# Kernel optimization log

Measured on AMD Instinct MI355X. Metric: run time of the kernel, lower is better.

Reference implementation:

```python
import jax, jax.numpy as jnp
import numpy as np

B, N, D = 8, 8192, 64          # batch, input points, point feature dim
NPOINT, NSAMPLE = 1024, 16     # FPS samples S, KNN neighbors K
WN, OUT = 16, 128              # weightnet out channels, output channels
CIN = 3 + D                    # concat(xyz_norm, point feats) = linear in_channel
NEG_SLOPE = 0.1


def setup_inputs() -> dict:
    key = jax.random.key(0)
    ks = jax.random.split(key, 8)
    rn = lambda k, shp, s: jax.random.normal(k, shp, jnp.float32) * s
    return {
        "xyz": rn(ks[0], (B, 3, N), 1.0),
        "points": rn(ks[1], (B, D, N), 1.0),
        "w1": rn(ks[2], (3, 8), 0.5), "b1": jnp.zeros((8,), jnp.float32),
        "w2": rn(ks[3], (8, 8), 0.35), "b2": jnp.zeros((8,), jnp.float32),
        "w3": rn(ks[4], (8, WN), 0.35), "b3": jnp.zeros((WN,), jnp.float32),
        "lin_w": rn(ks[5], (WN * CIN, OUT), 0.03),
        "lin_b": jnp.zeros((OUT,), jnp.float32),
    }


def _fps(xyz):
    """Furthest point sampling. xyz: [B,N,3] -> idx [B,NPOINT] int32."""
    def step(carry, _):
        dist, farthest = carry  # [B,N], [B]
        centroid = jnp.take_along_axis(xyz, farthest[:, None, None], axis=1)  # [B,1,3]
        d = jnp.sum((xyz - centroid) ** 2, axis=-1)  # [B,N]
        dist = jnp.minimum(dist, d)
        return (dist, jnp.argmax(dist, axis=-1).astype(jnp.int32)), farthest
    init = (jnp.full((xyz.shape[0], xyz.shape[1]), 1e10, xyz.dtype),
            jnp.zeros((xyz.shape[0],), jnp.int32))
    _, idxs = jax.lax.scan(step, init, None, length=NPOINT)
    return idxs.T  # [B, NPOINT]


def reference(xyz, points, w1, b1, w2, b2, w3, b3, lin_w, lin_b):
    xyz_t = xyz.transpose(0, 2, 1)       # [B,N,3]
    pts_t = points.transpose(0, 2, 1)    # [B,N,D]

    fps_idx = _fps(xyz_t)                                   # [B,S]
    bidx = jnp.arange(B)[:, None]
    new_xyz = xyz_t[bidx, fps_idx]                          # [B,S,3]

    # KNN: squared distances (same ordering as euclidean cdist)
    sqr = jnp.sum((new_xyz[:, :, None, :] - xyz_t[:, None, :, :]) ** 2, axis=-1)  # [B,S,N]
    _, knn = jax.lax.top_k(-sqr, NSAMPLE)                   # [B,S,K]

    b3i = jnp.arange(B)[:, None, None]
    g_xyz = xyz_t[b3i, knn]                                 # [B,S,K,3]
    g_xyz_norm = g_xyz - new_xyz[:, :, None, :]             # [B,S,K,3]
    g_pts = pts_t[b3i, knn]                                 # [B,S,K,D]
    feat = jnp.concatenate([g_xyz_norm, g_pts], axis=-1)    # [B,S,K,3+D]

    # WeightNet: 1x1 convs == per-neighbor MLP on xyz offsets
    h = jax.nn.relu(g_xyz_norm @ w1 + b1)
    h = jax.nn.relu(h @ w2 + b2)
    wts = jax.nn.relu(h @ w3 + b3)                          # [B,S,K,WN]

    # weighted aggregation over K, then flatten [C, WN]
    agg = jnp.einsum('bskc,bskw->bscw', feat, wts).reshape(B, NPOINT, CIN * WN)
    out = agg @ lin_w + lin_b                               # [B,S,OUT]
    out = jnp.where(out > 0, out, NEG_SLOPE * out)          # LeakyReLU(0.1)

    return new_xyz.transpose(0, 2, 1), out.transpose(0, 2, 1), fps_idx
```

## Files before the change

### kernel.cpp

```cpp
#include <hip/hip_runtime.h>
#include <hip/hip_bf16.h>

#define NPTS   8192
#define NBATCH 8
#define S      1024
#define K      16
#define D      64
#define CIN    67
#define WN     16
#define OUTC   128

#define OUT_MAIN 24576
#define OUT_FPS  1073152

#define T_FPS   0
#define T_TP    8
#define T_KNN   1032
#define T_FEAT  1544
#define T_GEMM  2568
#define NBLK    2824

typedef float v2f __attribute__((ext_vector_type(2)));

struct Ctrl {
  int ticket;
  int pad0[15];
  int progress[8];
  int knn_prefix[8];
  int tp_done[8];
  int pad1[8];
  int tile_done[128];
};

__device__ __forceinline__ void wait_ge(int* p, int need) {
  if (threadIdx.x == 0)
    while (__hip_atomic_load(p, __ATOMIC_ACQUIRE, __HIP_MEMORY_SCOPE_AGENT) < need)
      __builtin_amdgcn_s_sleep(2);
  __syncthreads();
}

template <int CTRL, int RM>
__device__ __forceinline__ unsigned long long dpp_max_step(unsigned long long key) {
  int lo = __builtin_amdgcn_update_dpp(0, (int)(unsigned)(key & 0xFFFFFFFFull), CTRL, RM, 0xF, true);
  int hi = __builtin_amdgcn_update_dpp(0, (int)(unsigned)(key >> 32),           CTRL, RM, 0xF, true);
  unsigned long long o = ((unsigned long long)(unsigned)hi << 32) | (unsigned)lo;
  return o > key ? o : key;
}

__device__ void fps_role(int b, const float* __restrict__ xyz, float4* __restrict__ nx4,
                         float* __restrict__ out, Ctrl* ctrl, void* smem)
{
#pragma clang fp contract(off)
  float* s_x = (float*)smem;
  float* s_y = s_x + NPTS;
  float* s_z = s_y + NPTS;
  float4* hist = (float4*)((char*)smem + 98304);
  unsigned long long* slots = (unsigned long long*)((char*)smem + 114688);

  const int tid  = threadIdx.x;
  const int wave = tid >> 6;
  const int lane = tid & 63;
  const float* xb = xyz + (size_t)b * 3 * NPTS;

  v2f px[8], py[8], pz[8], dist[8];
#pragma unroll
  for (int p = 0; p < 8; p++) {
    int ne = (2 * p) * 512 + tid;
    int no = ne + 512;
    px[p] = (v2f){xb[ne], xb[no]};
    py[p] = (v2f){xb[NPTS + ne], xb[NPTS + no]};
    pz[p] = (v2f){xb[2 * NPTS + ne], xb[2 * NPTS + no]};
    dist[p] = (v2f){1e10f, 1e10f};
    s_x[ne] = px[p].x; s_x[no] = px[p].y;
    s_y[ne] = py[p].x; s_y[no] = py[p].y;
    s_z[ne] = pz[p].x; s_z[no] = pz[p].y;
  }

  int far = 0;
  float cx = xb[0], cy = xb[NPTS], cz = xb[2 * NPTS];

  for (int t = 0; t < 1024; t++) {
    if (tid == (t & 511))
      hist[t] = make_float4(cx, cy, cz, (float)far);

    if ((t & 31) == 0 && t > 0 && wave == 0 && lane < 32) {
      int tt = t - 32 + lane;
      float4 h = hist[tt];
      nx4[(b << 10) + tt] = h;
      __threadfence();
      if (lane == 0)
        __hip_atomic_store(&ctrl->progress[b], t, __ATOMIC_RELEASE, __HIP_MEMORY_SCOPE_AGENT);
    }

    const v2f c2x = (v2f){cx, cx}, c2y = (v2f){cy, cy}, c2z = (v2f){cz, cz};

    float bd_e = -1.0f, bd_o = -1.0f;
    int   ce   = 0,     co   = 0;
#pragma unroll
    for (int p = 0; p < 8; p++) {
      v2f dx = px[p] - c2x, dy = py[p] - c2y, dz = pz[p] - c2z;
      v2f d  = (dx * dx + dy * dy) + dz * dz;
      float nde = fminf(dist[p].x, d.x);
      float ndo = fminf(dist[p].y, d.y);
      dist[p].x = nde;
      dist[p].y = ndo;
      if (nde > bd_e) { bd_e = nde; ce = 2 * p; }
      if (ndo > bd_o) { bd_o = ndo; co = 2 * p + 1; }
    }

    unsigned long long ke =
        ((unsigned long long)__float_as_uint(bd_e) << 32) | (unsigned)(~(unsigned)(ce * 512 + tid));
    unsigned long long ko =
        ((unsigned long long)__float_as_uint(bd_o) << 32) | (unsigned)(~(unsigned)(co * 512 + tid));
    unsigned long long key = ko > ke ? ko : ke;

    key = dpp_max_step<0x111, 0xF>(key);
    key = dpp_max_step<0x112, 0xF>(key);
    key = dpp_max_step<0x114, 0xF>(key);
    key = dpp_max_step<0x118, 0xF>(key);
    key = dpp_max_step<0x142, 0xA>(key);
    key = dpp_max_step<0x143, 0xC>(key);
    if (lane == 63) slots[(t & 1) * 8 + wave] = key;
    __syncthreads();

    const unsigned long long* sl = slots + (t & 1) * 8;
    unsigned long long k0 = sl[0], k1 = sl[1], k2 = sl[2], k3 = sl[3];
    unsigned long long k4 = sl[4], k5 = sl[5], k6 = sl[6], k7 = sl[7];
    k0 = k1 > k0 ? k1 : k0;
    k2 = k3 > k2 ? k3 : k2;
    k4 = k5 > k4 ? k5 : k4;
    k6 = k7 > k6 ? k7 : k6;
    k0 = k2 > k0 ? k2 : k0;
    k4 = k6 > k4 ? k6 : k4;
    k0 = k4 > k0 ? k4 : k0;
    int gi = (int)(~(unsigned)(k0 & 0xFFFFFFFFull));
    far = gi;
    cx = s_x[gi]; cy = s_y[gi]; cz = s_z[gi];
  }
  __syncthreads();

  if (wave == 0 && lane < 32) {
    int tt = 992 + lane;
    float4 h = hist[tt];
    nx4[(b << 10) + tt] = h;
    __threadfence();
    if (lane == 0)
      __hip_atomic_store(&ctrl->progress[b], 1024, __ATOMIC_RELEASE, __HIP_MEMORY_SCOPE_AGENT);
  }

#pragma unroll
  for (int j = 0; j < 2; j++) {
    int t = j * 512 + tid;
    float4 h = hist[t];
    out[OUT_FPS + b * 1024 + t] = h.w;
    out[b * 3072 + t]           = h.x;
    out[b * 3072 + 1024 + t]    = h.y;
    out[b * 3072 + 2048 + t]    = h.z;
  }
}

__device__ void tp_role(int bid, const float* __restrict__ pts, float* __restrict__ ptt,
                        Ctrl* ctrl, void* smem)
{
  float* tile = (float*)smem;
  const int b  = bid >> 7;
  const int n0 = (bid & 127) * 64;
  const float* pb = pts + (size_t)b * D * NPTS;
#pragma unroll
  for (int i = 0; i < 8; i++) {
    int s = threadIdx.x + i * 512;
    int nl = s & 63, d = s >> 6;
    tile[d * 65 + nl] = pb[(size_t)d * NPTS + n0 + nl];
  }
  __syncthreads();
  float* ob = ptt + ((size_t)b * NPTS + n0) * D;
#pragma unroll
  for (int i = 0; i < 8; i++) {
    int s = threadIdx.x + i * 512;
    int dl = s & 63, nl = s >> 6;
    ob[(size_t)nl * D + dl] = tile[dl * 65 + nl];
  }
  __syncthreads();
  if (threadIdx.x == 0) {
    __threadfence();
    __hip_atomic_fetch_add(&ctrl->tp_done[b], 1, __ATOMIC_RELEASE, __HIP_MEMORY_SCOPE_AGENT);
  }
}

__device__ void knn_role(int kidx, const float* __restrict__ xyz, const float4* __restrict__ nx4,
                         int* __restrict__ knn, Ctrl* ctrl, void* smem)
{
#pragma clang fp contract(off)
  unsigned long long (*s_k)[544] = (unsigned long long (*)[544])smem;
  const int tid   = threadIdx.x;
  const int cl    = tid >> 5;
  const int chunk = tid & 31;
  const int b     = kidx >> 6;
  const int c0    = (kidx & 63) * 16;
  const int csel  = (b << 10) + c0 + cl;

  wait_ge(&ctrl->progress[b], c0 + 16);

  const float* xb = xyz + (size_t)b * 3 * NPTS;
  const float4 c4 = nx4[csel];
  const float cx = c4.x, cy = c4.y, cz = c4.z;

  float nd[16]; int ni[16];
#pragma unroll
  for (int k = 0; k < 16; k++) { nd[k] = 3.4e38f; ni[k] = 0x7FFFFFFF; }

  for (int jj = 0; jj < 256; jj++) {
    int j = jj * 32 + chunk;
    float dx = xb[j] - cx, dy = xb[NPTS + j] - cy, dz = xb[2 * NPTS + j] - cz;
    float d  = (dx * dx + dy * dy) + dz * dz;
    float cv = d; int iv = j;
#pragma unroll
    for (int k = 0; k < 16; k++) {
      bool sw = cv < nd[k];
      float tv = nd[k]; int ti = ni[k];
      nd[k] = sw ? cv : tv;  ni[k] = sw ? iv : ti;
      cv    = sw ? tv : cv;  iv    = sw ? ti : iv;
    }
  }
#pragma unroll
  for (int k = 0; k < 16; k++)
    s_k[cl][chunk * 17 + k] =
        ((unsigned long long)__float_as_uint(nd[k]) << 32) | (unsigned)ni[k];
  s_k[cl][chunk * 17 + 16] = ~0ull;
  __syncthreads();

  if (tid < 16) {
    int pos[32];
#pragma unroll
    for (int c = 0; c < 32; c++) pos[c] = 0;
    for (int r = 0; r < 16; r++) {
      unsigned long long bk = ~0ull; int bc = 0;
#pragma unroll
      for (int c = 0; c < 32; c++) {
        unsigned long long kv = s_k[tid][c * 17 + pos[c]];
        if (kv < bk) { bk = kv; bc = c; }
      }
#pragma unroll
      for (int c = 0; c < 32; c++) pos[c] += (c == bc);
      knn[(size_t)((b << 10) + c0 + tid) * 16 + r] = (int)(bk & 0xFFFFFFFFull);
    }
  }
  __syncthreads();
  if (tid == 0) {
    __threadfence();
    while (__hip_atomic_load(&ctrl->knn_prefix[b], __ATOMIC_ACQUIRE, __HIP_MEMORY_SCOPE_AGENT) < c0)
      __builtin_amdgcn_s_sleep(2);
    __hip_atomic_store(&ctrl->knn_prefix[b], c0 + 16, __ATOMIC_RELEASE, __HIP_MEMORY_SCOPE_AGENT);
  }
}

__device__ void feat_role(int fidx, const float* __restrict__ xyz, const float4* __restrict__ nx4,
                          const float* __restrict__ ptt, const int* __restrict__ knn,
                          const float* __restrict__ w1, const float* __restrict__ b1,
                          const float* __restrict__ w2, const float* __restrict__ b2,
                          const float* __restrict__ w3, const float* __restrict__ b3,
                          float* __restrict__ agg, Ctrl* ctrl, void* smem)
{
  float* s_wts = (float*)smem;
  float* s_off = s_wts + 8 * 272;
  int*   s_nk  = (int*)(s_off + 8 * 48);

  const int C0 = fidx * 8;
  const int b  = C0 >> 10;
  const int c0l = C0 & 1023;

  wait_ge(&ctrl->knn_prefix[b], c0l + 8);
  wait_ge(&ctrl->tp_done[b], 128);

  const int wv   = threadIdx.x >> 6;
  const int lane = threadIdx.x & 63;
  const int csel = C0 + wv;

  if (lane < 16) {
    int nk = knn[(size_t)csel * 16 + lane];
    s_nk[wv * 16 + lane] = nk;
    const float* xb = xyz + (size_t)b * 3 * NPTS;
    const float4 c4 = nx4[csel];
    float ox = xb[nk]            - c4.x;
    float oy = xb[NPTS + nk]     - c4.y;
    float oz = xb[2 * NPTS + nk] - c4.z;
    s_off[wv * 48 + lane * 3 + 0] = ox;
    s_off[wv * 48 + lane * 3 + 1] = oy;
    s_off[wv * 48 + lane * 3 + 2] = oz;
    float h1[8], h2[8];
#pragma unroll
    for (int j = 0; j < 8; j++)
      h1[j] = fmaxf(0.f, ox * w1[j] + oy * w1[8 + j] + oz * w1[16 + j] + b1[j]);
#pragma unroll
    for (int j = 0; j < 8; j++) {
      float a = b2[j];
#pragma unroll
      for (int i = 0; i < 8; i++) a = fmaf(h1[i], w2[i * 8 + j], a);
      h2[j] = fmaxf(0.f, a);
    }
#pragma unroll
    for (int w = 0; w < 16; w++) {
      float a = b3[w];
#pragma unroll
      for (int i = 0; i < 8; i++) a = fmaf(h2[i], w3[i * 16 + w], a);
      s_wts[wv * 272 + lane * 17 + w] = fmaxf(0.f, a);
    }
  }
  __syncthreads();

  float f[16];
#pragma unroll
  for (int k = 0; k < 16; k++) {
    int nk = s_nk[wv * 16 + k];
    f[k] = ptt[((size_t)b * NPTS + nk) * D + lane];
  }

  float acc[16];
#pragma unroll
  for (int w = 0; w < 16; w++) acc[w] = 0.f;
#pragma unroll
  for (int k = 0; k < 16; k++) {
#pragma unroll
    for (int w = 0; w < 16; w++)
      acc[w] = fmaf(f[k], s_wts[wv * 272 + k * 17 + w], acc[w]);
  }
  float* arow = agg + (size_t)csel * (CIN * WN) + (3 + lane) * 16;
#pragma unroll
  for (int q = 0; q < 4; q++) {
    float4 v = make_float4(acc[4 * q], acc[4 * q + 1], acc[4 * q + 2], acc[4 * q + 3]);
    *(float4*)(arow + 4 * q) = v;
  }

  if (lane < 48) {
    int c = lane >> 4, w = lane & 15;
    float a = 0.f;
#pragma unroll
    for (int k = 0; k < 16; k++)
      a = fmaf(s_off[wv * 48 + k * 3 + c], s_wts[wv * 272 + k * 17 + w], a);
    agg[(size_t)csel * (CIN * WN) + c * 16 + w] = a;
  }
  __syncthreads();
  if (threadIdx.x == 0) {
    __threadfence();
    __hip_atomic_fetch_add(&ctrl->tile_done[C0 >> 6], 1, __ATOMIC_RELEASE, __HIP_MEMORY_SCOPE_AGENT);
  }
}

__device__ void gemm_role(int gidx, const float* __restrict__ agg, const float* __restrict__ lin_w,
                          const float* __restrict__ lin_b, float* __restrict__ out,
                          Ctrl* ctrl, void* smem)
{
  float* a_t = (float*)smem;
  float* b_t = a_t + 16 * 68;
  const int rt   = gidx >> 1;
  const int ct   = gidx & 1;
  const int row0 = rt * 64;
  const int c0   = ct * 64;

  wait_ge(&ctrl->tile_done[rt], 8);

  const int tid = threadIdx.x;
  const int cg  = tid & 31;
  const int rg  = tid >> 5;

  float acc[4][2] = {};
  for (int kt = 0; kt < 67; kt++) {
    const int k0 = kt * 16;
#pragma unroll
    for (int i = 0; i < 2; i++) {
      int s = tid + i * 512;
      int kk = s & 15, r = s >> 4;
      a_t[kk * 68 + r] = agg[(size_t)(row0 + r) * (CIN * WN) + k0 + kk];
    }
#pragma unroll
    for (int i = 0; i < 2; i++) {
      int s = tid + i * 512;
      int c = s & 63, kk = s >> 6;
      b_t[kk * 64 + c] = lin_w[(size_t)(k0 + kk) * OUTC + c0 + c];
    }
    __syncthreads();
#pragma unroll
    for (int kk = 0; kk < 16; kk++) {
      const float4 a0 = *(const float4*)&a_t[kk * 68 + rg * 4];
      float bv0 = b_t[kk * 64 + cg * 2];
      float bv1 = b_t[kk * 64 + cg * 2 + 1];
      float av[4] = {a0.x, a0.y, a0.z, a0.w};
#pragma unroll
      for (int rr = 0; rr < 4; rr++) {
        acc[rr][0] = fmaf(av[rr], bv0, acc[rr][0]);
        acc[rr][1] = fmaf(av[rr], bv1, acc[rr][1]);
      }
    }
    __syncthreads();
  }
#pragma unroll
  for (int rr = 0; rr < 4; rr++) {
#pragma unroll
    for (int cc = 0; cc < 2; cc++) {
      int R = row0 + rg * 4 + rr;
      int C = c0 + cg * 2 + cc;
      float v = acc[rr][cc] + lin_b[C];
      v = v > 0.f ? v : 0.1f * v;
      int bb = R >> 10, ss = R & 1023;
      out[OUT_MAIN + ((size_t)(bb * OUTC + C)) * 1024 + ss] = v;
    }
  }
}

__global__ __launch_bounds__(512)
void mega_kernel(const float* __restrict__ xyz, const float* __restrict__ pts,
                 const float* __restrict__ w1, const float* __restrict__ b1,
                 const float* __restrict__ w2, const float* __restrict__ b2,
                 const float* __restrict__ w3, const float* __restrict__ b3,
                 const float* __restrict__ lin_w, const float* __restrict__ lin_b,
                 float* __restrict__ out, float4* __restrict__ nx4,
                 int* __restrict__ knn, float* __restrict__ ptt,
                 float* __restrict__ agg, Ctrl* ctrl)
{
  __shared__ __align__(16) unsigned long long smem[14400];
  __shared__ int s_ticket;
  if (threadIdx.x == 0)
    s_ticket = __hip_atomic_fetch_add(&ctrl->ticket, 1, __ATOMIC_RELAXED, __HIP_MEMORY_SCOPE_AGENT);
  __syncthreads();
  const int tk = s_ticket;

  if (tk < T_TP)
    fps_role(tk, xyz, nx4, out, ctrl, smem);
  else if (tk < T_KNN)
    tp_role(tk - T_TP, pts, ptt, ctrl, smem);
  else if (tk < T_FEAT)
    knn_role(tk - T_KNN, xyz, nx4, knn, ctrl, smem);
  else if (tk < T_GEMM)
    feat_role(tk - T_FEAT, xyz, nx4, ptt, knn, w1, b1, w2, b2, w3, b3, agg, ctrl, smem);
  else
    gemm_role(tk - T_GEMM, agg, lin_w, lin_b, out, ctrl, smem);
}

extern "C" void kernel_launch(void* const* d_in, const int* in_sizes, int n_in,
                              void* d_out, int out_size, void* d_ws, size_t ws_size,
                              hipStream_t stream) {
  const float* xyz    = (const float*)d_in[0];
  const float* points = (const float*)d_in[1];
  const float* w1     = (const float*)d_in[2];
  const float* b1     = (const float*)d_in[3];
  const float* w2     = (const float*)d_in[4];
  const float* b2     = (const float*)d_in[5];
  const float* w3     = (const float*)d_in[6];
  const float* b3     = (const float*)d_in[7];
  const float* lin_w  = (const float*)d_in[8];
  const float* lin_b  = (const float*)d_in[9];
  float* out = (float*)d_out;
  char*  ws  = (char*)d_ws;

  float4* nx4  = (float4*)(ws);
  int*    knn  = (int*)   (ws + 131072);
  Ctrl*   ctrl = (Ctrl*)  (ws + 655360);
  float*  ptt  = (float*) (ws + 1048576);
  float*  agg  = (float*) (ws + 17825792);

  hipMemsetAsync(ctrl, 0, 4096, stream);
  mega_kernel<<<NBLK, 512, 0, stream>>>(xyz, points, w1, b1, w2, b2, w3, b3,
                                        lin_w, lin_b, out, nx4, knn, ptt, agg, ctrl);
}
```

Baseline: 1.543 ms.

## Replace progress counters with self-validating 64-bit data flags for FPS/KNN handoff

FPS results and KNN indices are now published as packed 64-bit relaxed atomic words with a nonzero sentinel (index+1), so consumers poll the data directly instead of waiting on progress counters and the serialized knn_prefix chain. This removes the thread fences and the in-order KNN prefix publication, letting feature blocks start as soon as their own neighbors are ready. The cost is a larger memset of the workspace, per-lane spinning on data, and reliance on relaxed atomics for ordering. Ordering on the nxA word relies on the x/y floats not both being zero, which is a subtle correctness risk.

```diff
diff --git a/kernel.cpp b/kernel.cpp
--- a/kernel.cpp
+++ b/kernel.cpp
@@ -20,22 +20,28 @@
 #define T_GEMM  2568
 #define NBLK    2824
 
+#define SCOPE __HIP_MEMORY_SCOPE_AGENT
+
 typedef float v2f __attribute__((ext_vector_type(2)));
 
 struct Ctrl {
   int ticket;
-  int pad0[15];
-  int progress[8];
-  int knn_prefix[8];
+  int pad0[31];
   int tp_done[8];
-  int pad1[8];
+  int pad1[24];
   int tile_done[128];
 };
 
-__device__ __forceinline__ void wait_ge(int* p, int need) {
+__device__ __forceinline__ unsigned long long aload64(const unsigned long long* p) {
+  return __hip_atomic_load(p, __ATOMIC_RELAXED, SCOPE);
+}
+__device__ __forceinline__ void astore64(unsigned long long* p, unsigned long long v) {
+  __hip_atomic_store(p, v, __ATOMIC_RELAXED, SCOPE);
+}
+__device__ __forceinline__ void wait_cnt(int* p, int need) {
   if (threadIdx.x == 0)
-    while (__hip_atomic_load(p, __ATOMIC_ACQUIRE, __HIP_MEMORY_SCOPE_AGENT) < need)
-      __builtin_amdgcn_s_sleep(2);
+    while (__hip_atomic_load(p, __ATOMIC_RELAXED, SCOPE) < need)
+      __builtin_amdgcn_s_sleep(4);
   __syncthreads();
 }
 
@@ -47,8 +53,10 @@
   return o > key ? o : key;
 }
 
-__device__ void fps_role(int b, const float* __restrict__ xyz, float4* __restrict__ nx4,
-                         float* __restrict__ out, Ctrl* ctrl, void* smem)
+__device__ void fps_role(int b, const float* __restrict__ xyz,
+                         unsigned long long* __restrict__ nxA,
+                         unsigned long long* __restrict__ nxB,
+                         float* __restrict__ out, void* smem)
 {
 #pragma clang fp contract(off)
   float* s_x = (float*)smem;
@@ -86,10 +94,11 @@
     if ((t & 31) == 0 && t > 0 && wave == 0 && lane < 32) {
       int tt = t - 32 + lane;
       float4 h = hist[tt];
-      nx4[(b << 10) + tt] = h;
-      __threadfence();
-      if (lane == 0)
-        __hip_atomic_store(&ctrl->progress[b], t, __ATOMIC_RELEASE, __HIP_MEMORY_SCOPE_AGENT);
+      int gidx = (b << 10) + tt;
+      astore64(&nxA[gidx],
+               ((unsigned long long)__float_as_uint(h.x) << 32) | __float_as_uint(h.y));
+      astore64(&nxB[gidx],
+               ((unsigned long long)__float_as_uint(h.z) << 32) | (unsigned)((int)h.w + 1));
     }
 
     const v2f c2x = (v2f){cx, cx}, c2y = (v2f){cy, cy}, c2z = (v2f){cz, cz};
@@ -142,10 +151,11 @@
   if (wave == 0 && lane < 32) {
     int tt = 992 + lane;
     float4 h = hist[tt];
-    nx4[(b << 10) + tt] = h;
-    __threadfence();
-    if (lane == 0)
-      __hip_atomic_store(&ctrl->progress[b], 1024, __ATOMIC_RELEASE, __HIP_MEMORY_SCOPE_AGENT);
+    int gidx = (b << 10) + tt;
+    astore64(&nxA[gidx],
+             ((unsigned long long)__float_as_uint(h.x) << 32) | __float_as_uint(h.y));
+    astore64(&nxB[gidx],
+             ((unsigned long long)__float_as_uint(h.z) << 32) | (unsigned)((int)h.w + 1));
   }
 
 #pragma unroll
@@ -181,29 +191,37 @@
     ob[(size_t)nl * D + dl] = tile[dl * 65 + nl];
   }
   __syncthreads();
-  if (threadIdx.x == 0) {
-    __threadfence();
-    __hip_atomic_fetch_add(&ctrl->tp_done[b], 1, __ATOMIC_RELEASE, __HIP_MEMORY_SCOPE_AGENT);
-  }
-}
-
-__device__ void knn_role(int kidx, const float* __restrict__ xyz, const float4* __restrict__ nx4,
-                         int* __restrict__ knn, Ctrl* ctrl, void* smem)
+  if (threadIdx.x == 0)
+    __hip_atomic_fetch_add(&ctrl->tp_done[b], 1, __ATOMIC_RELEASE, SCOPE);
+}
+
+__device__ void knn_role(int kidx, const float* __restrict__ xyz,
+                         const unsigned long long* __restrict__ nxA,
+                         const unsigned long long* __restrict__ nxB,
+                         unsigned long long* __restrict__ knnP, void* smem)
 {
 #pragma clang fp contract(off)
-  unsigned long long (*s_k)[544] = (unsigned long long (*)[544])smem;
+  float (*s_cc)[4] = (float(*)[4])smem;
+  unsigned long long* s_k = (unsigned long long*)((char*)smem + 256);
   const int tid   = threadIdx.x;
   const int cl    = tid >> 5;
   const int chunk = tid & 31;
   const int b     = kidx >> 6;
   const int c0    = (kidx & 63) * 16;
-  const int csel  = (b << 10) + c0 + cl;
-
-  wait_ge(&ctrl->progress[b], c0 + 16);
+  const int cbase = (b << 10) + c0;
+
+  if (chunk == 0) {
+    unsigned long long Bv, Av;
+    do { Bv = aload64(&nxB[cbase + cl]); } while ((unsigned)(Bv & 0xFFFFFFFFull) == 0u);
+    do { Av = aload64(&nxA[cbase + cl]); } while (Av == 0ull);
+    s_cc[cl][0] = __uint_as_float((unsigned)(Av >> 32));
+    s_cc[cl][1] = __uint_as_float((unsigned)(Av & 0xFFFFFFFFull));
+    s_cc[cl][2] = __uint_as_float((unsigned)(Bv >> 32));
+  }
+  __syncthreads();
 
   const float* xb = xyz + (size_t)b * 3 * NPTS;
-  const float4 c4 = nx4[csel];
-  const float cx = c4.x, cy = c4.y, cz = c4.z;
+  const float cx = s_cc[cl][0], cy = s_cc[cl][1], cz = s_cc[cl][2];
 
   float nd[16]; int ni[16];
 #pragma unroll
@@ -224,38 +242,40 @@
   }
 #pragma unroll
   for (int k = 0; k < 16; k++)
-    s_k[cl][chunk * 17 + k] =
+    s_k[cl * 545 + chunk * 17 + k] =
         ((unsigned long long)__float_as_uint(nd[k]) << 32) | (unsigned)ni[k];
-  s_k[cl][chunk * 17 + 16] = ~0ull;
+  s_k[cl * 545 + chunk * 17 + 16] = ~0ull;
   __syncthreads();
 
   if (tid < 16) {
     int pos[32];
 #pragma unroll
     for (int c = 0; c < 32; c++) pos[c] = 0;
+    int res[16];
     for (int r = 0; r < 16; r++) {
       unsigned long long bk = ~0ull; int bc = 0;
 #pragma unroll
       for (int c = 0; c < 32; c++) {
-        unsigned long long kv = s_k[tid][c * 17 + pos[c]];
+        unsigned long long kv = s_k[tid * 545 + c * 17 + pos[c]];
         if (kv < bk) { bk = kv; bc = c; }
       }
 #pragma unroll
       for (int c = 0; c < 32; c++) pos[c] += (c == bc);
-      knn[(size_t)((b << 10) + c0 + tid) * 16 + r] = (int)(bk & 0xFFFFFFFFull);
-    }
-  }
-  __syncthreads();
-  if (tid == 0) {
-    __threadfence();
-    while (__hip_atomic_load(&ctrl->knn_prefix[b], __ATOMIC_ACQUIRE, __HIP_MEMORY_SCOPE_AGENT) < c0)
-      __builtin_amdgcn_s_sleep(2);
-    __hip_atomic_store(&ctrl->knn_prefix[b], c0 + 16, __ATOMIC_RELEASE, __HIP_MEMORY_SCOPE_AGENT);
-  }
-}
-
-__device__ void feat_role(int fidx, const float* __restrict__ xyz, const float4* __restrict__ nx4,
-                          const float* __restrict__ ptt, const int* __restrict__ knn,
+      res[r] = (int)(bk & 0xFFFFFFFFull);
+    }
+#pragma unroll
+    for (int w = 0; w < 8; w++)
+      astore64(&knnP[(size_t)(cbase + tid) * 8 + w],
+               ((unsigned long long)(unsigned)(res[2 * w] + 1) << 32) |
+               (unsigned)(res[2 * w + 1] + 1));
+  }
+}
+
+__device__ void feat_role(int fidx, const float* __restrict__ xyz,
+                          const unsigned long long* __restrict__ nxA,
+                          const unsigned long long* __restrict__ nxB,
+                          const float* __restrict__ ptt,
+                          const unsigned long long* __restrict__ knnP,
                           const float* __restrict__ w1, const float* __restrict__ b1,
                           const float* __restrict__ w2, const float* __restrict__ b2,
                           const float* __restrict__ w3, const float* __restrict__ b3,
@@ -267,23 +287,32 @@
 
   const int C0 = fidx * 8;
   const int b  = C0 >> 10;
-  const int c0l = C0 & 1023;
-
-  wait_ge(&ctrl->knn_prefix[b], c0l + 8);
-  wait_ge(&ctrl->tp_done[b], 128);
+
+  wait_cnt(&ctrl->tp_done[b], 128);
 
   const int wv   = threadIdx.x >> 6;
   const int lane = threadIdx.x & 63;
   const int csel = C0 + wv;
 
   if (lane < 16) {
-    int nk = knn[(size_t)csel * 16 + lane];
+    const unsigned long long* wp = &knnP[(size_t)csel * 8 + (lane >> 1)];
+    unsigned long long wd;
+    do { wd = aload64(wp); } while (wd == 0ull);
+    unsigned v = (lane & 1) ? (unsigned)(wd & 0xFFFFFFFFull) : (unsigned)(wd >> 32);
+    int nk = (int)v - 1;
     s_nk[wv * 16 + lane] = nk;
+
+    unsigned long long Av, Bv;
+    do { Av = aload64(&nxA[csel]); } while (Av == 0ull);
+    do { Bv = aload64(&nxB[csel]); } while ((unsigned)(Bv & 0xFFFFFFFFull) == 0u);
+    float ccx = __uint_as_float((unsigned)(Av >> 32));
+    float ccy = __uint_as_float((unsigned)(Av & 0xFFFFFFFFull));
+    float ccz = __uint_as_float((unsigned)(Bv >> 32));
+
     const float* xb = xyz + (size_t)b * 3 * NPTS;
-    const float4 c4 = nx4[csel];
-    float ox = xb[nk]            - c4.x;
-    float oy = xb[NPTS + nk]     - c4.y;
-    float oz = xb[2 * NPTS + nk] - c4.z;
+    float ox = xb[nk]            - ccx;
+    float oy = xb[NPTS + nk]     - ccy;
+    float oz = xb[2 * NPTS + nk] - ccz;
     s_off[wv * 48 + lane * 3 + 0] = ox;
     s_off[wv * 48 + lane * 3 + 1] = oy;
     s_off[wv * 48 + lane * 3 + 2] = oz;
@@ -340,10 +369,8 @@
     agg[(size_t)csel * (CIN * WN) + c * 16 + w] = a;
   }
   __syncthreads();
-  if (threadIdx.x == 0) {
-    __threadfence();
-    __hip_atomic_fetch_add(&ctrl->tile_done[C0 >> 6], 1, __ATOMIC_RELEASE, __HIP_MEMORY_SCOPE_AGENT);
-  }
+  if (threadIdx.x == 0)
+    __hip_atomic_fetch_add(&ctrl->tile_done[C0 >> 6], 1, __ATOMIC_RELEASE, SCOPE);
 }
 
 __device__ void gemm_role(int gidx, const float* __restrict__ agg, const float* __restrict__ lin_w,
@@ -357,7 +384,7 @@
   const int row0 = rt * 64;
   const int c0   = ct * 64;
 
-  wait_ge(&ctrl->tile_done[rt], 8);
+  wait_cnt(&ctrl->tile_done[rt], 8);
 
   const int tid = threadIdx.x;
   const int cg  = tid & 31;
@@ -413,25 +440,26 @@
                  const float* __restrict__ w2, const float* __restrict__ b2,
                  const float* __restrict__ w3, const float* __restrict__ b3,
                  const float* __restrict__ lin_w, const float* __restrict__ lin_b,
-                 float* __restrict__ out, float4* __restrict__ nx4,
-                 int* __restrict__ knn, float* __restrict__ ptt,
-                 float* __restrict__ agg, Ctrl* ctrl)
+                 float* __restrict__ out, unsigned long long* __restrict__ nxA,
+                 unsigned long long* __restrict__ nxB, unsigned long long* __restrict__ knnP,
+                 float* __restrict__ ptt, float* __restrict__ agg, Ctrl* ctrl)
 {
   __shared__ __align__(16) unsigned long long smem[14400];
   __shared__ int s_ticket;
   if (threadIdx.x == 0)
-    s_ticket = __hip_atomic_fetch_add(&ctrl->ticket, 1, __ATOMIC_RELAXED, __HIP_MEMORY_SCOPE_AGENT);
+    s_ticket = __hip_atomic_fetch_add(&ctrl->ticket, 1, __ATOMIC_RELAXED, SCOPE);
   __syncthreads();
   const int tk = s_ticket;
 
   if (tk < T_TP)
-    fps_role(tk, xyz, nx4, out, ctrl, smem);
+    fps_role(tk, xyz, nxA, nxB, out, smem);
   else if (tk < T_KNN)
     tp_role(tk - T_TP, pts, ptt, ctrl, smem);
   else if (tk < T_FEAT)
-    knn_role(tk - T_KNN, xyz, nx4, knn, ctrl, smem);
+    knn_role(tk - T_KNN, xyz, nxA, nxB, knnP, smem);
   else if (tk < T_GEMM)
-    feat_role(tk - T_FEAT, xyz, nx4, ptt, knn, w1, b1, w2, b2, w3, b3, agg, ctrl, smem);
+    feat_role(tk - T_FEAT, xyz, nxA, nxB, ptt, knnP,
+              w1, b1, w2, b2, w3, b3, agg, ctrl, smem);
   else
     gemm_role(tk - T_GEMM, agg, lin_w, lin_b, out, ctrl, smem);
 }
@@ -452,13 +480,14 @@
   float* out = (float*)d_out;
   char*  ws  = (char*)d_ws;
 
-  float4* nx4  = (float4*)(ws);
-  int*    knn  = (int*)   (ws + 131072);
-  Ctrl*   ctrl = (Ctrl*)  (ws + 655360);
-  float*  ptt  = (float*) (ws + 1048576);
-  float*  agg  = (float*) (ws + 17825792);
-
-  hipMemsetAsync(ctrl, 0, 4096, stream);
+  Ctrl* ctrl                = (Ctrl*)(ws);
+  unsigned long long* nxA   = (unsigned long long*)(ws + 4096);
+  unsigned long long* nxB   = (unsigned long long*)(ws + 69632);
+  unsigned long long* knnP  = (unsigned long long*)(ws + 135168);
+  float* ptt                = (float*)(ws + 1048576);
+  float* agg                = (float*)(ws + 17825792);
+
+  hipMemsetAsync(ws, 0, 659456, stream);
   mega_kernel<<<NBLK, 512, 0, stream>>>(xyz, points, w1, b1, w2, b2, w3, b3,
-                                        lin_w, lin_b, out, nx4, knn, ptt, agg, ctrl);
-}
+                                        lin_w, lin_b, out, nxA, nxB, knnP, ptt, agg, ctrl);
+}
```

Measured after the change: 1.340 ms. 1.15x faster.
